# Performance work log

Measured on AMD Instinct MI355X. Metric: run time of the kernel, lower is better.

Reference implementation:

```python
import jax, jax.numpy as jnp
import numpy as np
import math

N, M, S, D = 256, 512, 128, 512  # num_vids, num_music, num_segments, embed_dim


def layer_norm(x, g, b, eps=1e-5):
    mu = jnp.mean(x, axis=-1, keepdims=True)
    var = jnp.mean(jnp.square(x - mu), axis=-1, keepdims=True)
    return (x - mu) * jax.lax.rsqrt(var + eps) * g + b


def setup_inputs() -> dict:
    key = jax.random.key(0)
    ks = jax.random.split(key, 16)
    s = 0.02
    return {
        "video_embeds": jax.random.normal(ks[0], (N, D), jnp.float32),
        "music_embeds": jax.random.normal(ks[1], (M, S, D), jnp.float32),
        "music_mask": jnp.ones((M, S), jnp.int32),
        "ln1_g": jnp.ones((D,), jnp.float32), "ln1_b": jnp.zeros((D,), jnp.float32),
        "Wq": jax.random.normal(ks[2], (D, D), jnp.float32) * s, "bq": jnp.zeros((D,), jnp.float32),
        "Wk": jax.random.normal(ks[3], (D, D), jnp.float32) * s, "bk": jnp.zeros((D,), jnp.float32),
        "Wv": jax.random.normal(ks[4], (D, D), jnp.float32) * s, "bv": jnp.zeros((D,), jnp.float32),
        "Wo": jax.random.normal(ks[5], (D, D), jnp.float32) * s, "bo": jnp.zeros((D,), jnp.float32),
        "Wl": jax.random.normal(ks[6], (D, D), jnp.float32) * s, "bl": jnp.zeros((D,), jnp.float32),
        "ln2_g": jnp.ones((D,), jnp.float32), "ln2_b": jnp.zeros((D,), jnp.float32),
        "ln3_g": jnp.ones((D,), jnp.float32), "ln3_b": jnp.zeros((D,), jnp.float32),
    }


def reference(video_embeds, music_embeds, music_mask,
              ln1_g, ln1_b, Wq, bq, Wk, bk, Wv, bv, Wo, bo, Wl, bl,
              ln2_g, ln2_b, ln3_g, ln3_b):
    d = video_embeds.shape[-1]
    # layer_norm1 applied to both streams
    v_ln = layer_norm(video_embeds, ln1_g, ln1_b)           # (N, D)
    m_ln = layer_norm(music_embeds, ln1_g, ln1_b)           # (M, S, D)
    # single-head cross-attention (MultiHeadedAttention_mask, num_heads=1)
    q = v_ln @ Wq.T + bq                                    # (N, D)
    k = m_ln @ Wk.T + bk                                    # (M, S, D)
    v = m_ln @ Wv.T + bv                                    # (M, S, D)
    logits = jnp.einsum('nd,msd->mns', q, k) / math.sqrt(d)  # (M, N, S)
    logits = jnp.where(music_mask[:, None, :] == 0, -jnp.inf, logits)
    weights = jax.nn.softmax(logits, axis=-1)               # softmax over segments
    attn = jnp.einsum('mns,msd->mnd', weights, v)           # (M, N, D)
    o = attn @ Wo.T + bo                                    # (M, N, D)
    # layer_norm2 -> linear -> residual (dropout is identity in eval) -> layer_norm3
    o = layer_norm(o, ln2_g, ln2_b)
    lin = o @ Wl.T + bl
    out = layer_norm(o + lin, ln3_g, ln3_b)
    return out
```

## Files before the change

kernel.cpp:

```cpp
#include <hip/hip_runtime.h>

typedef __attribute__((ext_vector_type(8))) short short8;
typedef __attribute__((ext_vector_type(4))) float f32x4;
typedef __attribute__((ext_vector_type(4))) unsigned short u16x4;

__device__ __forceinline__ unsigned short f2bf(float f){
  unsigned int u = __builtin_bit_cast(unsigned int, f);
  u = (u + 0x7FFFu + ((u >> 16) & 1u)) >> 16;
  return (unsigned short)u;
}
__device__ __forceinline__ float bf2f(unsigned short h){
  unsigned int u = ((unsigned int)h) << 16;
  return __builtin_bit_cast(float, u);
}
__device__ __forceinline__ f32x4 mfma16(short8 a, short8 b, f32x4 c){
  return __builtin_amdgcn_mfma_f32_16x16x32_bf16(a, b, c, 0, 0, 0);
}
__device__ __forceinline__ void gload16(const void* g, void* l){
  __builtin_amdgcn_global_load_lds((const __attribute__((address_space(1))) void*)g,
                                   (__attribute__((address_space(3))) void*)l, 16, 0, 0);
}

__global__ __launch_bounds__(256) void cvt_f32_bf16(const float* __restrict__ src,
                                                    unsigned short* __restrict__ dst){
  int i = (blockIdx.x * 256 + threadIdx.x) * 4;
  float4 v = *(const float4*)(src + i);
  u16x4 o = { f2bf(v.x), f2bf(v.y), f2bf(v.z), f2bf(v.w) };
  *(u16x4*)(dst + i) = o;
}

__global__ __launch_bounds__(256) void ln_rows(const float* __restrict__ x,
                                               const float* __restrict__ g,
                                               const float* __restrict__ b,
                                               unsigned short* __restrict__ y,
                                               int nrows){
  const int wid = threadIdx.x >> 6, lane = threadIdx.x & 63;
  const int row = blockIdx.x * 4 + wid;
  if (row >= nrows) return;
  const float* xr = x + (long)row * 512;
  float4 v0 = *(const float4*)(xr + lane * 4);
  float4 v1 = *(const float4*)(xr + 256 + lane * 4);
  float s  = v0.x + v0.y + v0.z + v0.w + v1.x + v1.y + v1.z + v1.w;
  float s2 = v0.x*v0.x + v0.y*v0.y + v0.z*v0.z + v0.w*v0.w
           + v1.x*v1.x + v1.y*v1.y + v1.z*v1.z + v1.w*v1.w;
  #pragma unroll
  for (int m = 1; m < 64; m <<= 1){ s += __shfl_xor(s, m); s2 += __shfl_xor(s2, m); }
  const float mu = s * (1.f/512.f);
  const float rstd = rsqrtf(s2 * (1.f/512.f) - mu*mu + 1e-5f);
  float4 g0 = *(const float4*)(g + lane*4), g1 = *(const float4*)(g + 256 + lane*4);
  float4 b0 = *(const float4*)(b + lane*4), b1 = *(const float4*)(b + 256 + lane*4);
  u16x4 o0 = { f2bf((v0.x-mu)*rstd*g0.x + b0.x), f2bf((v0.y-mu)*rstd*g0.y + b0.y),
               f2bf((v0.z-mu)*rstd*g0.z + b0.z), f2bf((v0.w-mu)*rstd*g0.w + b0.w) };
  u16x4 o1 = { f2bf((v1.x-mu)*rstd*g1.x + b1.x), f2bf((v1.y-mu)*rstd*g1.y + b1.y),
               f2bf((v1.z-mu)*rstd*g1.z + b1.z), f2bf((v1.w-mu)*rstd*g1.w + b1.w) };
  *(u16x4*)(y + (long)row * 512 + lane * 4) = o0;
  *(u16x4*)(y + (long)row * 512 + 256 + lane * 4) = o1;
}

__global__ __launch_bounds__(256) void ln_weight_prep(
    const float* __restrict__ Wl, const float* __restrict__ g2,
    const float* __restrict__ b2, const float* __restrict__ bl,
    const float* __restrict__ bo,
    unsigned short* __restrict__ wlp, float* __restrict__ u,
    float* __restrict__ v, float* __restrict__ bias_cat){
  const int wid = threadIdx.x >> 6, lane = threadIdx.x & 63;
  const int n = blockIdx.x * 4 + wid;
  const float* row = Wl + (long)n * 512;
  float su = 0.f, sv = 0.f, sc = 0.f;
  #pragma unroll
  for (int h = 0; h < 2; ++h){
    const int c0 = h * 256 + lane * 4;
    float4 w  = *(const float4*)(row + c0);
    float4 gg = *(const float4*)(g2 + c0);
    float4 bb = *(const float4*)(b2 + c0);
    float4 oo = *(const float4*)(bo + c0);
    float4 wp = { w.x*gg.x, w.y*gg.y, w.z*gg.z, w.w*gg.w };
    su += wp.x + wp.y + wp.z + wp.w;
    sv += w.x*bb.x + w.y*bb.y + w.z*bb.z + w.w*bb.w;
    sc += wp.x*oo.x + wp.y*oo.y + wp.z*oo.z + wp.w*oo.w;
    u16x4 o = { f2bf(wp.x), f2bf(wp.y), f2bf(wp.z), f2bf(wp.w) };
    *(u16x4*)(wlp + (long)n * 512 + c0) = o;
  }
  #pragma unroll
  for (int m = 1; m < 64; m <<= 1){
    su += __shfl_xor(su, m); sv += __shfl_xor(sv, m); sc += __shfl_xor(sc, m);
  }
  if (lane == 0){
    u[n] = su;
    v[n] = sv + bl[n];
    bias_cat[n] = bo[n];
    bias_cat[512 + n] = sc;
  }
}

__global__ __launch_bounds__(256) void transpose_bf(const float* __restrict__ src,
                                                    unsigned short* __restrict__ dst){
  __shared__ float tile[64][65];
  const int t = threadIdx.x;
  const int k0 = blockIdx.x * 64, c0 = blockIdx.y * 64;
  const int j = t & 63, i = t >> 6;
  #pragma unroll
  for (int rr = 0; rr < 16; ++rr)
    tile[i + rr*4][j] = src[(long)(c0 + i + rr*4) * 512 + k0 + j];
  __syncthreads();
  #pragma unroll
  for (int rr = 0; rr < 16; ++rr)
    dst[(long)(k0 + i + rr*4) * 512 + c0 + j] = f2bf(tile[j][i + rr*4]);
}

__global__ __launch_bounds__(256) void gemm_bt(const unsigned short* __restrict__ A,
                                               const unsigned short* __restrict__ B,
                                               const float* __restrict__ bias,
                                               unsigned short* __restrict__ out,
                                               int transposed){
  __shared__ unsigned short At[128][40];
  __shared__ unsigned short Bt[128][40];
  const int t = threadIdx.x, lane = t & 63, wid = t >> 6;
  const int l15 = lane & 15, l4 = lane >> 4;
  const int wr = wid >> 1, wc = wid & 1;
  const int rowBase = blockIdx.y * 128;
  const int colBase = blockIdx.x * 128;
  f32x4 zero = {0.f, 0.f, 0.f, 0.f};
  f32x4 acc[4][4];
  #pragma unroll
  for (int i = 0; i < 4; ++i)
    #pragma unroll
    for (int j = 0; j < 4; ++j) acc[i][j] = zero;
  const int sr = t >> 1, sh = (t & 1) * 16;
  for (int ks = 0; ks < 16; ++ks){
    const int k0 = ks * 32;
    const unsigned short* sa = A + (long)(rowBase + sr) * 512 + k0 + sh;
    *(short8*)&At[sr][sh]     = *(const short8*)sa;
    *(short8*)&At[sr][sh + 8] = *(const short8*)(sa + 8);
    const unsigned short* sb = B + (long)(colBase + sr) * 512 + k0 + sh;
    *(short8*)&Bt[sr][sh]     = *(const short8*)sb;
    *(short8*)&Bt[sr][sh + 8] = *(const short8*)(sb + 8);
    __syncthreads();
    short8 af[4], bfv[4];
    #pragma unroll
    for (int i = 0; i < 4; ++i) af[i]  = *(const short8*)&At[wr*64 + i*16 + l15][l4*8];
    #pragma unroll
    for (int i = 0; i < 4; ++i) bfv[i] = *(const short8*)&Bt[wc*64 + i*16 + l15][l4*8];
    #pragma unroll
    for (int i = 0; i < 4; ++i)
      #pragma unroll
      for (int j = 0; j < 4; ++j)
        acc[i][j] = mfma16(af[i], bfv[j], acc[i][j]);
    __syncthreads();
  }
  #pragma unroll
  for (int i = 0; i < 4; ++i){
    const int r0 = rowBase + wr*64 + i*16 + l4*4;
    #pragma unroll
    for (int j = 0; j < 4; ++j){
      const int c = colBase + wc*64 + j*16 + l15;
      const float bb = bias ? bias[c] : 0.f;
      #pragma unroll
      for (int jr = 0; jr < 4; ++jr){
        const float v = acc[i][j][jr] + bb;
        const long rr = r0 + jr;
        if (!transposed){
          out[rr * 512 + c] = f2bf(v);
        } else {
          const long m = rr >> 7, s = rr & 127;
          out[(m * 512 + c) * 128 + s] = f2bf(v);
        }
      }
    }
  }
}

__global__ __launch_bounds__(256) void gemm_kv97(const unsigned short* __restrict__ A,
                                                 const unsigned short* __restrict__ B,
                                                 const float* __restrict__ bk,
                                                 const float* __restrict__ bv,
                                                 unsigned short* __restrict__ kout,
                                                 unsigned short* __restrict__ vout){
  __shared__ unsigned short A_lds[4096];
  __shared__ unsigned short B_lds[4096];
  const int t = threadIdx.x, lane = t & 63, wid = t >> 6;
  const int l15 = lane & 15, l4 = lane >> 4;
  const int wr = wid >> 1, wc = wid & 1;
  const int b = blockIdx.x;
  const int kk = b >> 3;
  const int colBase = (kk & 7) * 128;
  const long panel = (b & 7) + 8 * (kk >> 3);
  const long rowBase = panel * 128;
  f32x4 zero = {0.f,0.f,0.f,0.f};
  f32x4 acc[4][4];
  #pragma unroll
  for (int i = 0; i < 4; ++i)
    #pragma unroll
    for (int j = 0; j < 4; ++j) acc[i][j] = zero;
  for (int ks = 0; ks < 16; ++ks){
    const int k0 = ks * 32;
    #pragma unroll
    for (int h = 0; h < 2; ++h){
      const int p = h*256 + t;
      const int row = p >> 2, g = (p & 3) ^ ((row >> 1) & 3);
      gload16(A + (rowBase + row)*512 + k0 + g*8, A_lds + p*8);
      gload16(B + (long)(colBase + row)*512 + k0 + g*8, B_lds + p*8);
    }
    __syncthreads();
    short8 af[4], bfv[4];
    #pragma unroll
    for (int i = 0; i < 4; ++i){
      const int ra = wr*64 + i*16 + l15;
      af[i]  = *(const short8*)(A_lds + (ra*4 + (l4 ^ ((ra >> 1) & 3)))*8);
      const int rb = wc*64 + i*16 + l15;
      bfv[i] = *(const short8*)(B_lds + (rb*4 + (l4 ^ ((rb >> 1) & 3)))*8);
    }
    #pragma unroll
    for (int i = 0; i < 4; ++i)
      #pragma unroll
      for (int j = 0; j < 4; ++j)
        acc[i][j] = mfma16(af[i], bfv[j], acc[i][j]);
    __syncthreads();
  }
  if (colBase < 512){
    #pragma unroll
    for (int i = 0; i < 4; ++i){
      const long r0 = rowBase + wr*64 + i*16 + l4*4;
      #pragma unroll
      for (int j = 0; j < 4; ++j){
        const int c = colBase + wc*64 + j*16 + l15;
        const float bb = bk[c];
        #pragma unroll
        for (int jr = 0; jr < 4; ++jr)
          kout[(r0 + jr)*512 + c] = f2bf(acc[i][j][jr] + bb);
      }
    }
  } else {
    #pragma unroll
    for (int i = 0; i < 4; ++i){
      const int s0 = wr*64 + i*16 + l4*4;
      #pragma unroll
      for (int j = 0; j < 4; ++j){
        const int d = colBase - 512 + wc*64 + j*16 + l15;
        const float bb = bv[d];
        #pragma unroll
        for (int jr = 0; jr < 4; ++jr)
          vout[(panel*512 + d)*128 + s0 + jr] = f2bf(acc[i][j][jr] + bb);
      }
    }
  }
}

__global__ __launch_bounds__(256) void attn_kernel(const unsigned short* __restrict__ q,
                                                   const unsigned short* __restrict__ k,
                                                   const unsigned short* __restrict__ vT,
                                                   const int* __restrict__ mask,
                                                   unsigned short* __restrict__ attn){
  __shared__ __align__(16) char smem[58880];
  unsigned short (*q_lds)[520] = (unsigned short (*)[520])smem;
  unsigned short* k_lin = (unsigned short*)(smem + 33280);
  float (*lg)[132]      = (float (*)[132])(smem + 33280);
  unsigned short (*w_lds)[136] = (unsigned short (*)[136])(smem + 50176);
  unsigned short* v_lin = (unsigned short*)smem;
  const int bq = blockIdx.x;
  const int m = (bq & 7) + 8 * ((bq >> 3) >> 3);
  const int nb = (bq >> 3) & 7;
  const int t = threadIdx.x, lane = t & 63, wid = t >> 6;
  const int l15 = lane & 15, l4 = lane >> 4;
  {
    const int r = t >> 3, c0 = (t & 7) * 64;
    const unsigned short* src = q + (long)(nb*32 + r) * 512 + c0;
    #pragma unroll
    for (int i = 0; i < 64; i += 8)
      *(short8*)&q_lds[r][c0 + i] = *(const short8*)(src + i);
  }
  f32x4 zero = {0.f,0.f,0.f,0.f};
  f32x4 acc[2][2];
  acc[0][0]=zero; acc[0][1]=zero; acc[1][0]=zero; acc[1][1]=zero;
  const unsigned short* kbase = k + (long)m * 128 * 512;
  for (int ks = 0; ks < 16; ++ks){
    const int k0 = ks * 32;
    #pragma unroll
    for (int h = 0; h < 2; ++h){
      const int p = h*256 + t;
      const int row = p >> 2, g = (p & 3) ^ ((row >> 1) & 3);
      gload16(kbase + (long)row*512 + k0 + g*8, k_lin + p*8);
    }
    __syncthreads();
    short8 af[2], bfv[2];
    #pragma unroll
    for (int i = 0; i < 2; ++i) af[i] = *(const short8*)&q_lds[i*16 + l15][k0 + l4*8];
    #pragma unroll
    for (int i = 0; i < 2; ++i){
      const int rb = wid*32 + i*16 + l15;
      bfv[i] = *(const short8*)(k_lin + (rb*4 + (l4 ^ ((rb >> 1) & 3)))*8);
    }
    #pragma unroll
    for (int i = 0; i < 2; ++i)
      #pragma unroll
      for (int j = 0; j < 2; ++j)
        acc[i][j] = mfma16(af[i], bfv[j], acc[i][j]);
    __syncthreads();
  }
  const float scale = 0.04419417382415922f;
  #pragma unroll
  for (int i = 0; i < 2; ++i)
    #pragma unroll
    for (int j = 0; j < 2; ++j)
      #pragma unroll
      for (int jr = 0; jr < 4; ++jr)
        lg[i*16 + l4*4 + jr][wid*32 + j*16 + l15] = acc[i][j][jr] * scale;
  __syncthreads();
  {
    const int row = t >> 3, u = t & 7;
    const int* mrow = mask + m * 128;
    float vals[16];
    float mx = -3.0e38f;
    #pragma unroll
    for (int i = 0; i < 16; ++i){
      const int s = u*16 + i;
      const float vv = (mrow[s] == 0) ? -3.0e38f : lg[row][s];
      vals[i] = vv;
      mx = fmaxf(mx, vv);
    }
    mx = fmaxf(mx, __shfl_xor(mx, 1));
    mx = fmaxf(mx, __shfl_xor(mx, 2));
    mx = fmaxf(mx, __shfl_xor(mx, 4));
    float sum = 0.f;
    #pragma unroll
    for (int i = 0; i < 16; ++i){
      const float e = __expf(vals[i] - mx);
      vals[i] = e;
      sum += e;
    }
    sum += __shfl_xor(sum, 1);
    sum += __shfl_xor(sum, 2);
    sum += __shfl_xor(sum, 4);
    const float inv = (sum > 0.f) ? (1.f / sum) : 0.f;
    #pragma unroll
    for (int i = 0; i < 16; i += 4){
      u16x4 o = { f2bf(vals[i]*inv), f2bf(vals[i+1]*inv),
                  f2bf(vals[i+2]*inv), f2bf(vals[i+3]*inv) };
      *(u16x4*)&w_lds[row][u*16 + i] = o;
    }
  }
  const long rowb = (long)m * 256 + nb * 32;
  const unsigned short* vbase = vT + (long)m * 512 * 128;
  for (int db = 0; db < 4; ++db){
    __syncthreads();
    #pragma unroll
    for (int it = 0; it < 8; ++it){
      const int p = it*256 + t;
      const int row = p >> 4, g = (p & 15) ^ (row & 7);
      gload16(vbase + (long)(db*128 + row)*128 + g*8, v_lin + p*8);
    }
    __syncthreads();
    f32x4 pacc[2][2];
    pacc[0][0]=zero; pacc[0][1]=zero; pacc[1][0]=zero; pacc[1][1]=zero;
    #pragma unroll
    for (int ks2 = 0; ks2 < 4; ++ks2){
      short8 wf[2], vf[2];
      #pragma unroll
      for (int i = 0; i < 2; ++i) wf[i] = *(const short8*)&w_lds[i*16 + l15][ks2*32 + l4*8];
      #pragma unroll
      for (int i = 0; i < 2; ++i){
        const int rv = wid*32 + i*16 + l15;
        vf[i] = *(const short8*)(v_lin + (rv*16 + ((ks2*4 + l4) ^ (rv & 7)))*8);
      }
      #pragma unroll
      for (int i = 0; i < 2; ++i)
        #pragma unroll
        for (int j = 0; j < 2; ++j)
          pacc[i][j] = mfma16(wf[i], vf[j], pacc[i][j]);
    }
    #pragma unroll
    for (int i = 0; i < 2; ++i)
      #pragma unroll
      for (int j = 0; j < 2; ++j)
        #pragma unroll
        for (int jr = 0; jr < 4; ++jr)
          attn[(rowb + i*16 + l4*4 + jr) * 512 + db*128 + wid*32 + j*16 + l15] =
              f2bf(pacc[i][j][jr]);
  }
}

__global__ __launch_bounds__(256) void gemm97(const unsigned short* __restrict__ A,
                                              const unsigned short* __restrict__ B,
                                              unsigned short* __restrict__ C){
  __shared__ unsigned short A_lds[4096];
  __shared__ unsigned short B_lds[4096];
  const int t = threadIdx.x, lane = t & 63, wid = t >> 6;
  const int l15 = lane & 15, l4 = lane >> 4;
  const int wr = wid >> 1, wc = wid & 1;
  const int b = blockIdx.x;
  const int kk = b >> 3;
  const int colBase = (kk & 7) * 128;
  const long rowBase = ((long)(b & 7) + 8 * (kk >> 3)) * 128;
  f32x4 zero = {0.f,0.f,0.f,0.f};
  f32x4 acc[4][4];
  #pragma unroll
  for (int i = 0; i < 4; ++i)
    #pragma unroll
    for (int j = 0; j < 4; ++j) acc[i][j] = zero;
  for (int ks = 0; ks < 16; ++ks){
    const int k0 = ks * 32;
    #pragma unroll
    for (int h = 0; h < 2; ++h){
      const int p = h*256 + t;
      const int row = p >> 2, g = (p & 3) ^ ((row >> 1) & 3);
      gload16(A + (rowBase + row)*512 + k0 + g*8, A_lds + p*8);
      gload16(B + (long)(colBase + row)*512 + k0 + g*8, B_lds + p*8);
    }
    __syncthreads();
    short8 af[4], bfv[4];
    #pragma unroll
    for (int i = 0; i < 4; ++i){
      const int ra = wr*64 + i*16 + l15;
      af[i]  = *(const short8*)(A_lds + (ra*4 + (l4 ^ ((ra >> 1) & 3)))*8);
      const int rb = wc*64 + i*16 + l15;
      bfv[i] = *(const short8*)(B_lds + (rb*4 + (l4 ^ ((rb >> 1) & 3)))*8);
    }
    #pragma unroll
    for (int i = 0; i < 4; ++i)
      #pragma unroll
      for (int j = 0; j < 4; ++j)
        acc[i][j] = mfma16(af[i], bfv[j], acc[i][j]);
    __syncthreads();
  }
  #pragma unroll
  for (int i = 0; i < 4; ++i){
    const long r0 = rowBase + wr*64 + i*16 + l4*4;
    #pragma unroll
    for (int j = 0; j < 4; ++j){
      const int c = colBase + wc*64 + j*16 + l15;
      #pragma unroll
      for (int jr = 0; jr < 4; ++jr)
        C[(r0 + jr)*1024 + c] = f2bf(acc[i][j][jr]);
    }
  }
}

__global__ __launch_bounds__(256) void ln_epilogue(
    const unsigned short* Cb, float* out,
    const float* __restrict__ bias_cat, const float* __restrict__ u,
    const float* __restrict__ v,
    const float* __restrict__ g2, const float* __restrict__ b2,
    const float* __restrict__ g3, const float* __restrict__ b3){
  const int wid = threadIdx.x >> 6, lane = threadIdx.x & 63;
  const long row = (long)blockIdx.x * 4 + wid;
  const unsigned short* cr = Cb + row * 1024;
  short8 ov = *(const short8*)(cr + lane * 8);
  short8 pv = *(const short8*)(cr + 512 + lane * 8);
  const int n0 = lane * 8;
  float4 bo0 = *(const float4*)(bias_cat + n0);
  float4 bo1 = *(const float4*)(bias_cat + n0 + 4);
  float4 c20 = *(const float4*)(bias_cat + 512 + n0);
  float4 c21 = *(const float4*)(bias_cat + 512 + n0 + 4);
  float o[8], p[8];
  #pragma unroll
  for (int j = 0; j < 4; ++j){
    o[j]   = bf2f((unsigned short)ov[j])   + ((const float*)&bo0)[j];
    o[4+j] = bf2f((unsigned short)ov[4+j]) + ((const float*)&bo1)[j];
    p[j]   = bf2f((unsigned short)pv[j])   + ((const float*)&c20)[j];
    p[4+j] = bf2f((unsigned short)pv[4+j]) + ((const float*)&c21)[j];
  }
  float s = 0.f, s2 = 0.f;
  #pragma unroll
  for (int j = 0; j < 8; ++j){ s += o[j]; s2 += o[j]*o[j]; }
  #pragma unroll
  for (int m = 1; m < 64; m <<= 1){ s += __shfl_xor(s, m); s2 += __shfl_xor(s2, m); }
  const float mu2 = s * (1.f/512.f);
  const float rstd2 = rsqrtf(s2 * (1.f/512.f) - mu2*mu2 + 1e-5f);
  float4 uv0 = *(const float4*)(u + n0), uv1 = *(const float4*)(u + n0 + 4);
  float4 vv0 = *(const float4*)(v + n0), vv1 = *(const float4*)(v + n0 + 4);
  float4 g20v = *(const float4*)(g2 + n0), g21v = *(const float4*)(g2 + n0 + 4);
  float4 b20v = *(const float4*)(b2 + n0), b21v = *(const float4*)(b2 + n0 + 4);
  float y[8];
  #pragma unroll
  for (int j = 0; j < 4; ++j){
    const float lin0 = rstd2 * (p[j]   - mu2 * ((const float*)&uv0)[j]) + ((const float*)&vv0)[j];
    const float lin1 = rstd2 * (p[4+j] - mu2 * ((const float*)&uv1)[j]) + ((const float*)&vv1)[j];
    const float oln0 = (o[j]   - mu2) * rstd2 * ((const float*)&g20v)[j] + ((const float*)&b20v)[j];
    const float oln1 = (o[4+j] - mu2) * rstd2 * ((const float*)&g21v)[j] + ((const float*)&b21v)[j];
    y[j]   = oln0 + lin0;
    y[4+j] = oln1 + lin1;
  }
  float t1 = 0.f, t2 = 0.f;
  #pragma unroll
  for (int j = 0; j < 8; ++j){ t1 += y[j]; t2 += y[j]*y[j]; }
  #pragma unroll
  for (int m = 1; m < 64; m <<= 1){ t1 += __shfl_xor(t1, m); t2 += __shfl_xor(t2, m); }
  const float mu3 = t1 * (1.f/512.f);
  const float rstd3 = rsqrtf(t2 * (1.f/512.f) - mu3*mu3 + 1e-5f);
  float4 g30v = *(const float4*)(g3 + n0), g31v = *(const float4*)(g3 + n0 + 4);
  float4 b30v = *(const float4*)(b3 + n0), b31v = *(const float4*)(b3 + n0 + 4);
  float4 r0, r1;
  #pragma unroll
  for (int j = 0; j < 4; ++j){
    ((float*)&r0)[j] = (y[j]   - mu3) * rstd3 * ((const float*)&g30v)[j] + ((const float*)&b30v)[j];
    ((float*)&r1)[j] = (y[4+j] - mu3) * rstd3 * ((const float*)&g31v)[j] + ((const float*)&b31v)[j];
  }
  *(float4*)(out + row * 512 + n0)     = r0;
  *(float4*)(out + row * 512 + n0 + 4) = r1;
}

extern "C" void kernel_launch(void* const* d_in, const int* in_sizes, int n_in,
                              void* d_out, int out_size, void* d_ws, size_t ws_size,
                              hipStream_t stream){
  const float* video = (const float*)d_in[0];
  const float* music = (const float*)d_in[1];
  const int*   mask  = (const int*)d_in[2];
  const float* ln1g  = (const float*)d_in[3];
  const float* ln1b  = (const float*)d_in[4];
  const float* Wq = (const float*)d_in[5];  const float* bq = (const float*)d_in[6];
  const float* Wk = (const float*)d_in[7];  const float* bk = (const float*)d_in[8];
  const float* Wv = (const float*)d_in[9];  const float* bv = (const float*)d_in[10];
  const float* Wo = (const float*)d_in[11]; const float* bo = (const float*)d_in[12];
  const float* Wl = (const float*)d_in[13]; const float* bl = (const float*)d_in[14];
  const float* g2 = (const float*)d_in[15]; const float* b2 = (const float*)d_in[16];
  const float* g3 = (const float*)d_in[17]; const float* b3 = (const float*)d_in[18];

  char* ob = (char*)d_out;
  unsigned short* mln   = (unsigned short*)ob;
  unsigned short* kbuf  = (unsigned short*)(ob + 67108864);
  unsigned short* vTbuf = (unsigned short*)(ob + 134217728);
  unsigned short* Cbuf  = (unsigned short*)ob;
  float* outp = (float*)d_out;

  char* wsb = (char*)d_ws;
  unsigned short* attnb = (unsigned short*)wsb;
  unsigned short* Wq_bf = (unsigned short*)(wsb + 134217728);
  unsigned short* KVcat = Wq_bf + 262144;
  unsigned short* q_ws  = KVcat + 524288;
  unsigned short* vln   = q_ws + 131072;
  unsigned short* Bcat  = vln + 131072;
  unsigned short* wlp   = Bcat + 524288;
  unsigned short* WoT   = wlp + 262144;
  float* bias_cat = (float*)(WoT + 262144);
  float* u_vec    = bias_cat + 1024;
  float* v_vec    = u_vec + 512;

  cvt_f32_bf16<<<256, 256, 0, stream>>>(Wq, Wq_bf);
  cvt_f32_bf16<<<256, 256, 0, stream>>>(Wk, KVcat);
  cvt_f32_bf16<<<256, 256, 0, stream>>>(Wv, KVcat + 262144);
  cvt_f32_bf16<<<256, 256, 0, stream>>>(Wo, Bcat);
  ln_weight_prep<<<128, 256, 0, stream>>>(Wl, g2, b2, bl, bo, wlp, u_vec, v_vec, bias_cat);
  transpose_bf<<<dim3(8, 8), 256, 0, stream>>>(Wo, WoT);
  gemm_bt<<<dim3(4, 4), 256, 0, stream>>>(wlp, WoT, nullptr, Bcat + 262144, 0);

  ln_rows<<<16384, 256, 0, stream>>>(music, ln1g, ln1b, mln, 65536);
  ln_rows<<<64,    256, 0, stream>>>(video, ln1g, ln1b, vln, 256);

  gemm_bt<<<dim3(4, 2), 256, 0, stream>>>(vln, Wq_bf, bq, q_ws, 0);
  gemm_kv97<<<4096, 256, 0, stream>>>(mln, KVcat, bk, bv, kbuf, vTbuf);

  attn_kernel<<<4096, 256, 0, stream>>>(q_ws, kbuf, vTbuf, mask, attnb);

  for (int c = 0; c < 4; ++c){
    const long rowoff = (long)c * 32768;
    gemm97<<<2048, 256, 0, stream>>>(attnb + rowoff*512, Bcat, Cbuf + rowoff*1024);
    ln_epilogue<<<8192, 256, 0, stream>>>(Cbuf + rowoff*1024, outp + rowoff*512,
                                          bias_cat, u_vec, v_vec, g2, b2, g3, b3);
  }
}
```

Baseline: 682.8 us.

## Double query tile per attention block and do softmax in registers

The attention kernel now handles 64 query rows per block instead of 32, so the grid halves and each K/V tile loaded into LDS is reused across twice as many queries. The softmax is computed straight from the MFMA accumulators, using cross-lane shuffles plus a small cross-wave max/sum exchange in LDS, instead of spilling the logits to LDS and re-reading them. Normalization is deferred: unnormalized exponentials go into the weight matrix and the 1/sum factor is applied to the PV output. This cuts K/V global traffic and LDS round trips, but raises LDS use to about 73KB and adds accumulator registers, which may lower occupancy.

Result: faster. 659.4 us (-3.4%).

```diff
diff --git a/kernel.cpp b/kernel.cpp
--- a/kernel.cpp
+++ b/kernel.cpp
@@ -251,27 +251,28 @@
                                                    const unsigned short* __restrict__ vT,
                                                    const int* __restrict__ mask,
                                                    unsigned short* __restrict__ attn){
-  __shared__ __align__(16) char smem[58880];
+  __shared__ __align__(16) char smem[74752];
   unsigned short (*q_lds)[520] = (unsigned short (*)[520])smem;
-  unsigned short* k_lin = (unsigned short*)(smem + 33280);
-  float (*lg)[132]      = (float (*)[132])(smem + 33280);
-  unsigned short (*w_lds)[136] = (unsigned short (*)[136])(smem + 50176);
-  unsigned short* v_lin = (unsigned short*)smem;
-  const int bq = blockIdx.x;
-  const int m = (bq & 7) + 8 * ((bq >> 3) >> 3);
-  const int nb = (bq >> 3) & 7;
+  unsigned short* k_lin = (unsigned short*)(smem + 66560);
+  unsigned short (*w_lds)[136] = (unsigned short (*)[136])smem;
+  float* red = (float*)(smem + 17408);
+  unsigned short* v_lin = (unsigned short*)(smem + 19456);
+  const int b = blockIdx.x;
+  const int m = (b & 7) + 8 * ((b >> 3) >> 2);
+  const int qb = (b >> 3) & 3;
   const int t = threadIdx.x, lane = t & 63, wid = t >> 6;
   const int l15 = lane & 15, l4 = lane >> 4;
   {
-    const int r = t >> 3, c0 = (t & 7) * 64;
-    const unsigned short* src = q + (long)(nb*32 + r) * 512 + c0;
-    #pragma unroll
-    for (int i = 0; i < 64; i += 8)
+    const int r = t >> 2, c0 = (t & 3) * 128;
+    const unsigned short* src = q + (long)(qb*64 + r) * 512 + c0;
+    #pragma unroll
+    for (int i = 0; i < 128; i += 8)
       *(short8*)&q_lds[r][c0 + i] = *(const short8*)(src + i);
   }
   f32x4 zero = {0.f,0.f,0.f,0.f};
-  f32x4 acc[2][2];
-  acc[0][0]=zero; acc[0][1]=zero; acc[1][0]=zero; acc[1][1]=zero;
+  f32x4 acc[4][2];
+  #pragma unroll
+  for (int i = 0; i < 4; ++i){ acc[i][0] = zero; acc[i][1] = zero; }
   const unsigned short* kbase = k + (long)m * 128 * 512;
   for (int ks = 0; ks < 16; ++ks){
     const int k0 = ks * 32;
@@ -282,64 +283,75 @@
       gload16(kbase + (long)row*512 + k0 + g*8, k_lin + p*8);
     }
     __syncthreads();
-    short8 af[2], bfv[2];
-    #pragma unroll
-    for (int i = 0; i < 2; ++i) af[i] = *(const short8*)&q_lds[i*16 + l15][k0 + l4*8];
-    #pragma unroll
-    for (int i = 0; i < 2; ++i){
-      const int rb = wid*32 + i*16 + l15;
-      bfv[i] = *(const short8*)(k_lin + (rb*4 + (l4 ^ ((rb >> 1) & 3)))*8);
-    }
-    #pragma unroll
-    for (int i = 0; i < 2; ++i)
+    short8 af[4], bfv[2];
+    #pragma unroll
+    for (int i = 0; i < 4; ++i) af[i] = *(const short8*)&q_lds[i*16 + l15][k0 + l4*8];
+    #pragma unroll
+    for (int j = 0; j < 2; ++j){
+      const int rb = wid*32 + j*16 + l15;
+      bfv[j] = *(const short8*)(k_lin + (rb*4 + (l4 ^ ((rb >> 1) & 3)))*8);
+    }
+    #pragma unroll
+    for (int i = 0; i < 4; ++i)
       #pragma unroll
       for (int j = 0; j < 2; ++j)
         acc[i][j] = mfma16(af[i], bfv[j], acc[i][j]);
     __syncthreads();
   }
   const float scale = 0.04419417382415922f;
-  #pragma unroll
-  for (int i = 0; i < 2; ++i)
-    #pragma unroll
-    for (int j = 0; j < 2; ++j)
-      #pragma unroll
-      for (int jr = 0; jr < 4; ++jr)
-        lg[i*16 + l4*4 + jr][wid*32 + j*16 + l15] = acc[i][j][jr] * scale;
+  const int* mrow = mask + m * 128;
+  const int mk0 = mrow[wid*32 + l15];
+  const int mk1 = mrow[wid*32 + 16 + l15];
+  float e[4][2][4], wmax[4][4], wsum[4][4];
+  #pragma unroll
+  for (int i = 0; i < 4; ++i)
+    #pragma unroll
+    for (int jr = 0; jr < 4; ++jr){
+      float v0 = mk0 ? acc[i][0][jr]*scale : -3.0e38f;
+      float v1 = mk1 ? acc[i][1][jr]*scale : -3.0e38f;
+      float mx = fmaxf(v0, v1);
+      mx = fmaxf(mx, __shfl_xor(mx, 1));
+      mx = fmaxf(mx, __shfl_xor(mx, 2));
+      mx = fmaxf(mx, __shfl_xor(mx, 4));
+      mx = fmaxf(mx, __shfl_xor(mx, 8));
+      const float e0 = __expf(v0 - mx), e1 = __expf(v1 - mx);
+      float sm = e0 + e1;
+      sm += __shfl_xor(sm, 1);
+      sm += __shfl_xor(sm, 2);
+      sm += __shfl_xor(sm, 4);
+      sm += __shfl_xor(sm, 8);
+      e[i][0][jr] = e0; e[i][1][jr] = e1;
+      wmax[i][jr] = mx; wsum[i][jr] = sm;
+    }
+  if (l15 == 0){
+    #pragma unroll
+    for (int i = 0; i < 4; ++i)
+      #pragma unroll
+      for (int jr = 0; jr < 4; ++jr){
+        const int r = i*16 + l4*4 + jr;
+        red[r*8 + wid*2]     = wmax[i][jr];
+        red[r*8 + wid*2 + 1] = wsum[i][jr];
+      }
+  }
   __syncthreads();
-  {
-    const int row = t >> 3, u = t & 7;
-    const int* mrow = mask + m * 128;
-    float vals[16];
-    float mx = -3.0e38f;
-    #pragma unroll
-    for (int i = 0; i < 16; ++i){
-      const int s = u*16 + i;
-      const float vv = (mrow[s] == 0) ? -3.0e38f : lg[row][s];
-      vals[i] = vv;
-      mx = fmaxf(mx, vv);
-    }
-    mx = fmaxf(mx, __shfl_xor(mx, 1));
-    mx = fmaxf(mx, __shfl_xor(mx, 2));
-    mx = fmaxf(mx, __shfl_xor(mx, 4));
-    float sum = 0.f;
-    #pragma unroll
-    for (int i = 0; i < 16; ++i){
-      const float e = __expf(vals[i] - mx);
-      vals[i] = e;
-      sum += e;
-    }
-    sum += __shfl_xor(sum, 1);
-    sum += __shfl_xor(sum, 2);
-    sum += __shfl_xor(sum, 4);
-    const float inv = (sum > 0.f) ? (1.f / sum) : 0.f;
-    #pragma unroll
-    for (int i = 0; i < 16; i += 4){
-      u16x4 o = { f2bf(vals[i]*inv), f2bf(vals[i+1]*inv),
-                  f2bf(vals[i+2]*inv), f2bf(vals[i+3]*inv) };
-      *(u16x4*)&w_lds[row][u*16 + i] = o;
-    }
-  }
-  const long rowb = (long)m * 256 + nb * 32;
+  float inv[4][4];
+  #pragma unroll
+  for (int i = 0; i < 4; ++i)
+    #pragma unroll
+    for (int jr = 0; jr < 4; ++jr){
+      const int r = i*16 + l4*4 + jr;
+      float4 a = *(const float4*)(red + r*8);
+      float4 c = *(const float4*)(red + r*8 + 4);
+      const float gm = fmaxf(fmaxf(a.x, a.z), fmaxf(c.x, c.z));
+      const float gs = a.y*__expf(a.x - gm) + a.w*__expf(a.z - gm)
+                     + c.y*__expf(c.x - gm) + c.w*__expf(c.z - gm);
+      inv[i][jr] = (gs > 0.f) ? (1.f / gs) : 0.f;
+      const float sc = __expf(wmax[i][jr] - gm);
+      #pragma unroll
+      for (int j = 0; j < 2; ++j)
+        w_lds[r][wid*32 + j*16 + l15] = f2bf(e[i][j][jr] * sc);
+    }
+  const long rowb = (long)m * 256 + qb * 64;
   const unsigned short* vbase = vT + (long)m * 512 * 128;
   for (int db = 0; db < 4; ++db){
     __syncthreads();
@@ -350,32 +362,33 @@
       gload16(vbase + (long)(db*128 + row)*128 + g*8, v_lin + p*8);
     }
     __syncthreads();
-    f32x4 pacc[2][2];
-    pacc[0][0]=zero; pacc[0][1]=zero; pacc[1][0]=zero; pacc[1][1]=zero;
+    f32x4 pacc[4][2];
+    #pragma unroll
+    for (int i = 0; i < 4; ++i){ pacc[i][0] = zero; pacc[i][1] = zero; }
     #pragma unroll
     for (int ks2 = 0; ks2 < 4; ++ks2){
-      short8 wf[2], vf[2];
-      #pragma unroll
-      for (int i = 0; i < 2; ++i) wf[i] = *(const short8*)&w_lds[i*16 + l15][ks2*32 + l4*8];
-      #pragma unroll
-      for (int i = 0; i < 2; ++i){
-        const int rv = wid*32 + i*16 + l15;
-        vf[i] = *(const short8*)(v_lin + (rv*16 + ((ks2*4 + l4) ^ (rv & 7)))*8);
+      short8 wf[4], vf[2];
+      #pragma unroll
+      for (int i = 0; i < 4; ++i) wf[i] = *(const short8*)&w_lds[i*16 + l15][ks2*32 + l4*8];
+      #pragma unroll
+      for (int j = 0; j < 2; ++j){
+        const int rv = wid*32 + j*16 + l15;
+        vf[j] = *(const short8*)(v_lin + (rv*16 + ((ks2*4 + l4) ^ (rv & 7)))*8);
       }
       #pragma unroll
-      for (int i = 0; i < 2; ++i)
+      for (int i = 0; i < 4; ++i)
         #pragma unroll
         for (int j = 0; j < 2; ++j)
           pacc[i][j] = mfma16(wf[i], vf[j], pacc[i][j]);
     }
     #pragma unroll
-    for (int i = 0; i < 2; ++i)
+    for (int i = 0; i < 4; ++i)
       #pragma unroll
       for (int j = 0; j < 2; ++j)
         #pragma unroll
         for (int jr = 0; jr < 4; ++jr)
           attn[(rowb + i*16 + l4*4 + jr) * 512 + db*128 + wid*32 + j*16 + l15] =
-              f2bf(pacc[i][j][jr]);
+              f2bf(pacc[i][j][jr] * inv[i][jr]);
   }
 }
 
@@ -549,7 +562,7 @@
   gemm_bt<<<dim3(4, 2), 256, 0, stream>>>(vln, Wq_bf, bq, q_ws, 0);
   gemm_kv97<<<4096, 256, 0, stream>>>(mln, KVcat, bk, bv, kbuf, vTbuf);
 
-  attn_kernel<<<4096, 256, 0, stream>>>(q_ws, kbuf, vTbuf, mask, attnb);
+  attn_kernel<<<2048, 256, 0, stream>>>(q_ws, kbuf, vTbuf, mask, attnb);
 
   for (int c = 0; c < 4; ++c){
     const long rowoff = (long)c * 32768;
```
